# Optimization experiments

Hardware: AMD Instinct MI355X
Metric: run time of the kernel (lower is better)

Reference implementation:

```python
import jax, jax.numpy as jnp
import numpy as np
import math

B, C, H, W = 4, 256, 64, 64
N_GROUPS = 32
D_K = 64
N_HEADS = C // D_K  # 4
EPS = 1e-5


def setup_inputs() -> dict:
    key = jax.random.key(0)
    ks = jax.random.split(key, 7)
    return {
        "x": jax.random.normal(ks[0], (B, C, H, W), dtype=jnp.float32),
        "gamma": jax.random.uniform(ks[1], (C,), dtype=jnp.float32),
        "beta": jax.random.normal(ks[2], (C,), dtype=jnp.float32) * 0.1,
        "W_qkv": jax.random.normal(ks[3], (C, N_HEADS * D_K * 3), dtype=jnp.float32) * 0.02,
        "b_qkv": jax.random.normal(ks[4], (N_HEADS * D_K * 3,), dtype=jnp.float32) * 0.02,
        "W_out": jax.random.normal(ks[5], (N_HEADS * D_K, C), dtype=jnp.float32) * 0.02,
        "b_out": jax.random.normal(ks[6], (C,), dtype=jnp.float32) * 0.02,
    }


def _group_norm(x, gamma, beta):
    # x: [B, C, H, W], 32 groups, biased variance, eps=1e-5 (torch GroupNorm defaults)
    b, c, h, w = x.shape
    xg = x.reshape(b, N_GROUPS, c // N_GROUPS, h, w)
    mean = jnp.mean(xg, axis=(2, 3, 4), keepdims=True)
    var = jnp.var(xg, axis=(2, 3, 4), keepdims=True)
    xn = (xg - mean) / jnp.sqrt(var + EPS)
    xn = xn.reshape(b, c, h, w)
    return xn * gamma[None, :, None, None] + beta[None, :, None, None]


def reference(x, gamma, beta, W_qkv, b_qkv, W_out, b_out):
    b, c, h, w = x.shape
    n = h * w
    scale = 1.0 / math.sqrt(math.sqrt(D_K))
    # norm -> [B, N, C]
    hid = _group_norm(x, gamma, beta).reshape(b, c, n).transpose(0, 2, 1)
    # qkv projection -> [B, N, n_heads, 3*d_k], chunk on last dim
    qkv = (hid @ W_qkv + b_qkv).reshape(b, n, N_HEADS, 3 * D_K)
    q, k, v = jnp.split(qkv, 3, axis=-1)  # each [B, N, H, d_k]
    attn = jnp.einsum('bihd,bjhd->bijh', q * scale, k * scale)
    attn = jax.nn.softmax(attn, axis=2)  # softmax over j (keys)
    res = jnp.einsum('bijh,bjhd->bihd', attn, v).reshape(b, n, N_HEADS * D_K)
    res = res @ W_out + b_out  # [B, N, C]
    res = res.transpose(0, 2, 1).reshape(b, c, h, w)
    return (res + x) / math.sqrt(2.0)
```

## Files before the change

### kernel.cpp

```cpp
#include <hip/hip_runtime.h>
#include <math.h>

typedef float  f32x4   __attribute__((ext_vector_type(4)));
typedef float  f32x16  __attribute__((ext_vector_type(16)));
typedef __bf16 bf16x8  __attribute__((ext_vector_type(8)));
typedef __bf16 bf16x4  __attribute__((ext_vector_type(4)));

#define MFMA16(a, b, c) __builtin_amdgcn_mfma_f32_16x16x32_bf16((a), (b), (c), 0, 0, 0)
#define MFMA32(a, b, c) __builtin_amdgcn_mfma_f32_32x32x16_bf16((a), (b), (c), 0, 0, 0)

typedef __attribute__((address_space(3))) unsigned int lds_u32;
typedef __attribute__((address_space(1))) const unsigned int glb_u32;

__device__ __forceinline__ void gload16(const __bf16* g, char* l) {
    __builtin_amdgcn_global_load_lds((glb_u32*)g, (lds_u32*)l, 16, 0, 0);
}

static constexpr int BATCH = 4;
static constexpr int CH    = 256;
static constexpr int M_TOT = BATCH * 4096;

static constexpr float QSCALE = 0.18033688011112042f;

static constexpr size_t OFF_WQKV  = 0;
static constexpr size_t OFF_WOUT  = 196608ull * 2;
static constexpr size_t OFF_STATS = OFF_WOUT + 65536ull * 2;
static constexpr size_t OFF_HID   = OFF_STATS + 1024;
static constexpr size_t OFF_Q     = OFF_HID + (size_t)M_TOT * CH * 2;
static constexpr size_t OFF_K     = OFF_Q   + (size_t)M_TOT * CH * 2;
static constexpr size_t OFF_V     = OFF_K   + (size_t)M_TOT * CH * 2;

__global__ __launch_bounds__(256) void pre_kernel(const float* __restrict__ x,
                                                  float2* __restrict__ stats,
                                                  const float* __restrict__ wq,
                                                  const float* __restrict__ wo,
                                                  __bf16* __restrict__ wqf,
                                                  __bf16* __restrict__ wof) {
    if (blockIdx.x < 128) {
        int bg = blockIdx.x;
        const float4* p = (const float4*)(x + (size_t)bg * 32768);
        float s = 0.f, ss = 0.f;
        for (int i = threadIdx.x; i < 8192; i += 256) {
            float4 v = p[i];
            s  += (v.x + v.y) + (v.z + v.w);
            ss += v.x * v.x + v.y * v.y + v.z * v.z + v.w * v.w;
        }
#pragma unroll
        for (int d = 32; d > 0; d >>= 1) { s += __shfl_down(s, d); ss += __shfl_down(ss, d); }
        __shared__ float sh[8];
        int w = threadIdx.x >> 6, l = threadIdx.x & 63;
        if (l == 0) { sh[w] = s; sh[4 + w] = ss; }
        __syncthreads();
        if (threadIdx.x == 0) {
            float S = sh[0] + sh[1] + sh[2] + sh[3];
            float SS = sh[4] + sh[5] + sh[6] + sh[7];
            float mean = S * (1.f / 32768.f);
            float var  = SS * (1.f / 32768.f) - mean * mean;
            stats[bg] = make_float2(mean, rsqrtf(var + 1e-5f));
        }
    } else {
        int i = (blockIdx.x - 128) * 256 + threadIdx.x;
        if (i < 196608) {
            int e = i & 7, l = (i >> 3) & 63, kk = (i >> 9) & 7, jt = i >> 12;
            int kidx = kk * 32 + ((l >> 4) << 3) + e;
            int n = jt * 16 + (l & 15);
            wqf[i] = (__bf16)wq[kidx * 768 + n];
        } else {
            int i2 = i - 196608;
            int e = i2 & 7, l = (i2 >> 3) & 63, kk = (i2 >> 9) & 7, jt = i2 >> 12;
            int kidx = kk * 32 + ((l >> 4) << 3) + e;
            int n = jt * 16 + (l & 15);
            wof[i2] = (__bf16)wo[kidx * 256 + n];
        }
    }
}

__global__ __launch_bounds__(256) void gn_apply(const float* __restrict__ x,
                                                const float* __restrict__ gamma,
                                                const float* __restrict__ beta,
                                                const float2* __restrict__ stats,
                                                __bf16* __restrict__ hid) {
    int b  = blockIdx.x >> 6;
    int n0 = (blockIdx.x & 63) << 6;
    int c  = threadIdx.x;
    float2 st = stats[b * 32 + (c >> 3)];
    float gm = gamma[c] * st.y;
    float bt = beta[c] - st.x * gm;
    const float* xp = x + ((size_t)(b * 256 + c)) * 4096 + n0;
    __bf16* hp = hid + ((size_t)(b * 4096 + n0)) * 256 + c;
#pragma unroll
    for (int j4 = 0; j4 < 16; ++j4) {
        float4 v = *(const float4*)(xp + j4 * 4);
        hp[(size_t)(j4 * 4 + 0) * 256] = (__bf16)(v.x * gm + bt);
        hp[(size_t)(j4 * 4 + 1) * 256] = (__bf16)(v.y * gm + bt);
        hp[(size_t)(j4 * 4 + 2) * 256] = (__bf16)(v.z * gm + bt);
        hp[(size_t)(j4 * 4 + 3) * 256] = (__bf16)(v.w * gm + bt);
    }
}

__global__ __launch_bounds__(256) void qkv_gemm(const __bf16* __restrict__ hid,
                                                const __bf16* __restrict__ wf,
                                                const float* __restrict__ bqkv,
                                                __bf16* __restrict__ qb,
                                                __bf16* __restrict__ kb,
                                                __bf16* __restrict__ vb) {
    const int mt = blockIdx.x, nt = blockIdx.y;
    const int tid = threadIdx.x;
    const int w = tid >> 6, l = tid & 63;
    const int lr = l & 15, lh = l >> 4;
    f32x4 acc[4] = {{0.f,0.f,0.f,0.f},{0.f,0.f,0.f,0.f},{0.f,0.f,0.f,0.f},{0.f,0.f,0.f,0.f}};
    const __bf16* ap = hid + (size_t)(mt * 64 + w * 16 + lr) * 256 + lh * 8;
#pragma unroll
    for (int kk = 0; kk < 8; ++kk) {
        bf16x8 a = *(const bf16x8*)(ap + kk * 32);
#pragma unroll
        for (int fj = 0; fj < 4; ++fj) {
            bf16x8 bf = *(const bf16x8*)(wf + (size_t)(((nt * 4 + fj) * 8 + kk) * 64 + l) * 8);
            acc[fj] = MFMA16(a, bf, acc[fj]);
        }
    }
    const int part = nt % 3;
    const int head = nt / 3;
    const int b  = mt >> 6;
    const int n0 = (mt & 63) * 64;

    if (part == 2) {
        __shared__ float tile[64][72];
#pragma unroll
        for (int fj = 0; fj < 4; ++fj) {
            float bias = bqkv[head * 192 + 128 + fj * 16 + lr];
#pragma unroll
            for (int r = 0; r < 4; ++r)
                tile[w * 16 + lh * 4 + r][fj * 16 + lr] = acc[fj][r] + bias;
        }
        __syncthreads();
        int dd = tid >> 2, nq = tid & 3;
        __bf16* dstrow = vb + ((size_t)((b * 4 + head) * 64 + dd)) * 4096 + n0 + nq * 16;
        bf16x8 w0, w1;
#pragma unroll
        for (int cc = 0; cc < 8; ++cc) {
            int nl0 = nq * 16 + 8 * ((cc >> 2) & 1) + 4 * (cc >> 3) + (cc & 3);
            int cc1 = cc + 8;
            int nl1 = nq * 16 + 8 * ((cc1 >> 2) & 1) + 4 * (cc1 >> 3) + (cc1 & 3);
            w0[cc] = (__bf16)tile[nl0][dd];
            w1[cc] = (__bf16)tile[nl1][dd];
        }
        *(bf16x8*)dstrow = w0;
        *(bf16x8*)(dstrow + 8) = w1;
    } else {
        __bf16* dst = (part == 0) ? qb : kb;
        const float sc = (part == 0) ? QSCALE : 1.0f;
        int mbase = w * 16 + lh * 4;
#pragma unroll
        for (int fj = 0; fj < 4; ++fj) {
            int dd = fj * 16 + lr;
            float bias = bqkv[head * 192 + part * 64 + dd];
#pragma unroll
            for (int r = 0; r < 4; ++r) {
                int n = n0 + mbase + r;
                dst[((size_t)((b * 4 + head) * 4096 + n)) * 64 + dd] = (__bf16)((acc[fj][r] + bias) * sc);
            }
        }
    }
}

__global__ __launch_bounds__(256, 2) void attn_fwd(const __bf16* __restrict__ q,
                                                   const __bf16* __restrict__ k,
                                                   const __bf16* __restrict__ vt,
                                                   __bf16* __restrict__ ao) {
    const int id = blockIdx.x;
    const int within = id >> 3;
    const int bh = ((id & 7) << 1) + (within >> 5);
    const int q0 = (within & 31) * 128;
    const int tid = threadIdx.x;
    const int wv = tid >> 6, l = tid & 63;
    const int l31 = l & 31, h = l >> 5;

    __shared__ __attribute__((aligned(16))) char smem[32768];

    const size_t base = (size_t)bh * (4096 * 64);

    const int c0 = wv * 64 + l;
    const int rK = c0 >> 3, cbK = l & 7;
    const int gk0 = rK * 64 + (cbK ^ (rK & 7)) * 8;
    const int gk1 = gk0 + 2048;
    const int gv0 = rK * 4096 + (cbK ^ (rK & 7)) * 8;
    const int gv1 = gv0 + 32 * 4096;
    const int lw0 = wv * 1024;
    const int lw1 = 4096 + wv * 1024;

    const __bf16* kg = k + base;
    const __bf16* vg = vt + base;

    int foff[2][4];
#pragma unroll
    for (int b32 = 0; b32 < 2; ++b32) {
        int row = b32 * 32 + l31;
#pragma unroll
        for (int s = 0; s < 4; ++s)
            foff[b32][s] = row * 128 + ((s * 32 + h * 16) ^ ((row & 7) << 4));
    }

    bf16x8 qf[4];
    {
        const __bf16* qp = q + base + (size_t)(q0 + wv * 32 + l31) * 64 + h * 8;
#pragma unroll
        for (int ks = 0; ks < 4; ++ks) qf[ks] = *(const bf16x8*)(qp + ks * 16);
    }
    bf16x8 ones;
#pragma unroll
    for (int e = 0; e < 8; ++e) ones[e] = (__bf16)1.0f;

    f32x16 O0 = (f32x16)0.0f, O1 = (f32x16)0.0f, LS = (f32x16)0.0f;

    gload16(kg + gk0, smem + lw0);
    gload16(kg + gk1, smem + lw1);
    gload16(vg + gv0, smem + 16384 + lw0);
    gload16(vg + gv1, smem + 16384 + lw1);
    __syncthreads();

    auto body = [&](const char* Kc, const char* Vc, char* kd, char* vd, int tnext) {
        if (tnext < 64) {
            const __bf16* kp = kg + (size_t)tnext * 4096;
            const __bf16* vp = vg + (size_t)tnext * 64;
            gload16(kp + gk0, kd + lw0);
            gload16(kp + gk1, kd + lw1);
            gload16(vp + gv0, vd + lw0);
            gload16(vp + gv1, vd + lw1);
        }

        f32x16 S0 = (f32x16)0.0f, S1 = (f32x16)0.0f;
        __builtin_amdgcn_s_setprio(1);
#pragma unroll
        for (int ks = 0; ks < 4; ++ks) {
            bf16x8 ka0 = *(const bf16x8*)(Kc + foff[0][ks]);
            bf16x8 ka1 = *(const bf16x8*)(Kc + foff[1][ks]);
            S0 = MFMA32(ka0, qf[ks], S0);
            S1 = MFMA32(ka1, qf[ks], S1);
        }
        __builtin_amdgcn_s_setprio(0);

        bf16x8 B0, B1, B2, B3;
#pragma unroll
        for (int e = 0; e < 8; ++e) {
            B0[e] = (__bf16)__builtin_amdgcn_exp2f(S0[e]);
            B1[e] = (__bf16)__builtin_amdgcn_exp2f(S0[8 + e]);
            B2[e] = (__bf16)__builtin_amdgcn_exp2f(S1[e]);
            B3[e] = (__bf16)__builtin_amdgcn_exp2f(S1[8 + e]);
        }

        __builtin_amdgcn_s_setprio(1);
        {
            bf16x8 v00 = *(const bf16x8*)(Vc + foff[0][0]);
            bf16x8 v10 = *(const bf16x8*)(Vc + foff[1][0]);
            O0 = MFMA32(v00, B0, O0);
            O1 = MFMA32(v10, B0, O1);
            LS = MFMA32(ones, B0, LS);
            bf16x8 v01 = *(const bf16x8*)(Vc + foff[0][1]);
            bf16x8 v11 = *(const bf16x8*)(Vc + foff[1][1]);
            O0 = MFMA32(v01, B1, O0);
            O1 = MFMA32(v11, B1, O1);
            LS = MFMA32(ones, B1, LS);
            bf16x8 v02 = *(const bf16x8*)(Vc + foff[0][2]);
            bf16x8 v12 = *(const bf16x8*)(Vc + foff[1][2]);
            O0 = MFMA32(v02, B2, O0);
            O1 = MFMA32(v12, B2, O1);
            LS = MFMA32(ones, B2, LS);
            bf16x8 v03 = *(const bf16x8*)(Vc + foff[0][3]);
            bf16x8 v13 = *(const bf16x8*)(Vc + foff[1][3]);
            O0 = MFMA32(v03, B3, O0);
            O1 = MFMA32(v13, B3, O1);
            LS = MFMA32(ones, B3, LS);
        }
        __builtin_amdgcn_s_setprio(0);

        __syncthreads();
    };

    for (int t = 0; t < 64; t += 2) {
        body(smem,        smem + 16384,        smem + 8192, smem + 16384 + 8192, t + 1);
        body(smem + 8192, smem + 16384 + 8192, smem,        smem + 16384,        t + 2);
    }

    float inv = 1.0f / LS[0];
    int b = bh >> 2, hd = bh & 3;
    int n = q0 + wv * 32 + l31;
    __bf16* dst = ao + ((size_t)(b * 4096 + n)) * 256 + hd * 64 + h * 4;
#pragma unroll
    for (int dt = 0; dt < 2; ++dt) {
        const f32x16& O = dt ? O1 : O0;
#pragma unroll
        for (int g = 0; g < 4; ++g) {
            bf16x4 pk;
#pragma unroll
            for (int m = 0; m < 4; ++m) pk[m] = (__bf16)(O[g * 4 + m] * inv);
            *(bf16x4*)(dst + dt * 32 + g * 8) = pk;
        }
    }
}

__global__ __launch_bounds__(256) void out_gemm(const __bf16* __restrict__ ao,
                                                const __bf16* __restrict__ wf,
                                                const float* __restrict__ bout,
                                                const float* __restrict__ x,
                                                float* __restrict__ out) {
    const int mt = blockIdx.x, nt = blockIdx.y;
    const int tid = threadIdx.x;
    const int w = tid >> 6, l = tid & 63;
    const int lr = l & 15, lh = l >> 4;
    f32x4 acc[4] = {{0.f,0.f,0.f,0.f},{0.f,0.f,0.f,0.f},{0.f,0.f,0.f,0.f},{0.f,0.f,0.f,0.f}};
    const __bf16* ap = ao + (size_t)(mt * 64 + w * 16 + lr) * 256 + lh * 8;
#pragma unroll
    for (int kk = 0; kk < 8; ++kk) {
        bf16x8 a = *(const bf16x8*)(ap + kk * 32);
#pragma unroll
        for (int fj = 0; fj < 4; ++fj) {
            bf16x8 bf = *(const bf16x8*)(wf + (size_t)(((nt * 4 + fj) * 8 + kk) * 64 + l) * 8);
            acc[fj] = MFMA16(a, bf, acc[fj]);
        }
    }
    __shared__ float tile[64][72];
#pragma unroll
    for (int fj = 0; fj < 4; ++fj) {
        float bias = bout[nt * 64 + fj * 16 + lr];
#pragma unroll
        for (int r = 0; r < 4; ++r)
            tile[w * 16 + lh * 4 + r][fj * 16 + lr] = acc[fj][r] + bias;
    }
    __syncthreads();
    int b  = mt >> 6;
    int n0 = (mt & 63) * 64;
    int c0 = nt * 64;
    int cl = tid >> 2, nq = tid & 3;
    size_t gbase = ((size_t)(b * 256 + c0 + cl)) * 4096 + n0 + nq * 16;
#pragma unroll
    for (int i = 0; i < 16; i += 4) {
        float4 xv = *(const float4*)(x + gbase + i);
        float4 ov;
        ov.x = (tile[nq * 16 + i + 0][cl] + xv.x) * 0.70710678118654752f;
        ov.y = (tile[nq * 16 + i + 1][cl] + xv.y) * 0.70710678118654752f;
        ov.z = (tile[nq * 16 + i + 2][cl] + xv.z) * 0.70710678118654752f;
        ov.w = (tile[nq * 16 + i + 3][cl] + xv.w) * 0.70710678118654752f;
        *(float4*)(out + gbase + i) = ov;
    }
}

extern "C" void kernel_launch(void* const* d_in, const int* in_sizes, int n_in,
                              void* d_out, int out_size, void* d_ws, size_t ws_size,
                              hipStream_t stream) {
    const float* x     = (const float*)d_in[0];
    const float* gamma = (const float*)d_in[1];
    const float* beta  = (const float*)d_in[2];
    const float* W_qkv = (const float*)d_in[3];
    const float* b_qkv = (const float*)d_in[4];
    const float* W_out = (const float*)d_in[5];
    const float* b_out = (const float*)d_in[6];
    float* out = (float*)d_out;
    char* ws = (char*)d_ws;

    __bf16* wqf   = (__bf16*)(ws + OFF_WQKV);
    __bf16* wof   = (__bf16*)(ws + OFF_WOUT);
    float2* stats = (float2*)(ws + OFF_STATS);
    __bf16* hid   = (__bf16*)(ws + OFF_HID);
    __bf16* qb    = (__bf16*)(ws + OFF_Q);
    __bf16* kb    = (__bf16*)(ws + OFF_K);
    __bf16* vbt   = (__bf16*)(ws + OFF_V);

    pre_kernel<<<1152, 256, 0, stream>>>(x, stats, W_qkv, W_out, wqf, wof);
    gn_apply<<<256, 256, 0, stream>>>(x, gamma, beta, stats, hid);
    qkv_gemm<<<dim3(256, 12), 256, 0, stream>>>(hid, wqf, b_qkv, qb, kb, vbt);
    attn_fwd<<<512, 256, 0, stream>>>(qb, kb, vbt, hid);
    out_gemm<<<dim3(256, 4), 256, 0, stream>>>(hid, wof, b_out, x, out);
}
```

Baseline: 144.4 us.

## Split attention key range across wave pairs and merge partial outputs in LDS

Each attention block now handles 64 queries instead of 128. Its four waves form two pairs, and each pair processes half of the keys with its own double-buffered K/V tiles. The launch doubles to 1024 blocks with a larger occupancy target, and the ones-matrix MFMA row sum is replaced by scalar accumulation of the exponentials. At the end, partial O and row sums are reduced through shared memory. This trades more blocks and an extra LDS reduction step for more parallelism and fewer MFMAs per tile, and it drops the LDS swizzle, which may add bank conflicts.

```diff
diff --git a/kernel.cpp b/kernel.cpp
--- a/kernel.cpp
+++ b/kernel.cpp
@@ -164,137 +164,130 @@
     }
 }
 
-__global__ __launch_bounds__(256, 2) void attn_fwd(const __bf16* __restrict__ q,
+__global__ __launch_bounds__(256, 4) void attn_fwd(const __bf16* __restrict__ q,
                                                    const __bf16* __restrict__ k,
                                                    const __bf16* __restrict__ vt,
                                                    __bf16* __restrict__ ao) {
     const int id = blockIdx.x;
     const int within = id >> 3;
-    const int bh = ((id & 7) << 1) + (within >> 5);
-    const int q0 = (within & 31) * 128;
+    const int bh = ((id & 7) << 1) + (within >> 6);
+    const int q0 = (within & 63) * 64;
     const int tid = threadIdx.x;
     const int wv = tid >> 6, l = tid & 63;
     const int l31 = l & 31, h = l >> 5;
+    const int pair = wv >> 1;
+    const int wq   = wv & 1;
 
     __shared__ __attribute__((aligned(16))) char smem[32768];
 
     const size_t base = (size_t)bh * (4096 * 64);
-
-    const int c0 = wv * 64 + l;
-    const int rK = c0 >> 3, cbK = l & 7;
-    const int gk0 = rK * 64 + (cbK ^ (rK & 7)) * 8;
-    const int gk1 = gk0 + 2048;
-    const int gv0 = rK * 4096 + (cbK ^ (rK & 7)) * 8;
-    const int gv1 = gv0 + 32 * 4096;
-    const int lw0 = wv * 1024;
-    const int lw1 = 4096 + wv * 1024;
-
     const __bf16* kg = k + base;
     const __bf16* vg = vt + base;
 
-    int foff[2][4];
-#pragma unroll
-    for (int b32 = 0; b32 < 2; ++b32) {
-        int row = b32 * 32 + l31;
-#pragma unroll
-        for (int s = 0; s < 4; ++s)
-            foff[b32][s] = row * 128 + ((s * 32 + h * 16) ^ ((row & 7) << 4));
-    }
+    const int kS0 = (l & 31) * 64 + wq * 16 + (l >> 5) * 8;
+    const int kS1 = kS0 + 32;
+    const int vS0 = (l & 31) * 4096 + wq * 16 + (l >> 5) * 8;
+    const int vS1 = vS0 + 32 * 4096;
+    const int dst0 = wq * 1024 + l * 16;
+    const int dst1 = dst0 + 2048;
+    const int pairBase = pair * 16384;
+    const int kTileStride = 2048;
+    const int pairKeyElemsK = pair * 131072;
+    const int pairColV = pair * 2048;
 
     bf16x8 qf[4];
     {
-        const __bf16* qp = q + base + (size_t)(q0 + wv * 32 + l31) * 64 + h * 8;
+        const __bf16* qp = q + base + (size_t)(q0 + wq * 32 + l31) * 64 + h * 8;
 #pragma unroll
         for (int ks = 0; ks < 4; ++ks) qf[ks] = *(const bf16x8*)(qp + ks * 16);
     }
-    bf16x8 ones;
-#pragma unroll
-    for (int e = 0; e < 8; ++e) ones[e] = (__bf16)1.0f;
-
-    f32x16 O0 = (f32x16)0.0f, O1 = (f32x16)0.0f, LS = (f32x16)0.0f;
-
-    gload16(kg + gk0, smem + lw0);
-    gload16(kg + gk1, smem + lw1);
-    gload16(vg + gv0, smem + 16384 + lw0);
-    gload16(vg + gv1, smem + 16384 + lw1);
+
+    f32x16 O0 = (f32x16)0.0f, O1 = (f32x16)0.0f;
+    float ls = 0.f;
+
+    gload16(kg + pairKeyElemsK + kS0, smem + pairBase + dst0);
+    gload16(kg + pairKeyElemsK + kS1, smem + pairBase + dst1);
+    gload16(vg + pairColV + vS0, smem + pairBase + 8192 + dst0);
+    gload16(vg + pairColV + vS1, smem + pairBase + 8192 + dst1);
     __syncthreads();
 
-    auto body = [&](const char* Kc, const char* Vc, char* kd, char* vd, int tnext) {
+    auto body = [&](int buf, int tnext) {
         if (tnext < 64) {
-            const __bf16* kp = kg + (size_t)tnext * 4096;
-            const __bf16* vp = vg + (size_t)tnext * 64;
-            gload16(kp + gk0, kd + lw0);
-            gload16(kp + gk1, kd + lw1);
-            gload16(vp + gv0, vd + lw0);
-            gload16(vp + gv1, vd + lw1);
-        }
-
-        f32x16 S0 = (f32x16)0.0f, S1 = (f32x16)0.0f;
+            const __bf16* kp = kg + pairKeyElemsK + tnext * kTileStride;
+            const __bf16* vp = vg + pairColV + tnext * 32;
+            char* kd = smem + pairBase + (buf ^ 1) * 4096;
+            char* vd = smem + pairBase + 8192 + (buf ^ 1) * 4096;
+            gload16(kp + kS0, kd + dst0);
+            gload16(kp + kS1, kd + dst1);
+            gload16(vp + vS0, vd + dst0);
+            gload16(vp + vS1, vd + dst1);
+        }
+        const char* Kl = smem + pairBase + buf * 4096 + l * 16;
+        const char* Vl = smem + pairBase + 8192 + buf * 4096 + l * 16;
+
+        f32x16 S = (f32x16)0.0f;
         __builtin_amdgcn_s_setprio(1);
 #pragma unroll
-        for (int ks = 0; ks < 4; ++ks) {
-            bf16x8 ka0 = *(const bf16x8*)(Kc + foff[0][ks]);
-            bf16x8 ka1 = *(const bf16x8*)(Kc + foff[1][ks]);
-            S0 = MFMA32(ka0, qf[ks], S0);
-            S1 = MFMA32(ka1, qf[ks], S1);
-        }
+        for (int ks = 0; ks < 4; ++ks)
+            S = MFMA32(*(const bf16x8*)(Kl + ks * 1024), qf[ks], S);
         __builtin_amdgcn_s_setprio(0);
 
-        bf16x8 B0, B1, B2, B3;
+        bf16x8 B0, B1;
 #pragma unroll
         for (int e = 0; e < 8; ++e) {
-            B0[e] = (__bf16)__builtin_amdgcn_exp2f(S0[e]);
-            B1[e] = (__bf16)__builtin_amdgcn_exp2f(S0[8 + e]);
-            B2[e] = (__bf16)__builtin_amdgcn_exp2f(S1[e]);
-            B3[e] = (__bf16)__builtin_amdgcn_exp2f(S1[8 + e]);
+            float p0 = __builtin_amdgcn_exp2f(S[e]);
+            float p1 = __builtin_amdgcn_exp2f(S[8 + e]);
+            ls += p0 + p1;
+            B0[e] = (__bf16)p0;
+            B1[e] = (__bf16)p1;
         }
 
         __builtin_amdgcn_s_setprio(1);
-        {
-            bf16x8 v00 = *(const bf16x8*)(Vc + foff[0][0]);
-            bf16x8 v10 = *(const bf16x8*)(Vc + foff[1][0]);
-            O0 = MFMA32(v00, B0, O0);
-            O1 = MFMA32(v10, B0, O1);
-            LS = MFMA32(ones, B0, LS);
-            bf16x8 v01 = *(const bf16x8*)(Vc + foff[0][1]);
-            bf16x8 v11 = *(const bf16x8*)(Vc + foff[1][1]);
-            O0 = MFMA32(v01, B1, O0);
-            O1 = MFMA32(v11, B1, O1);
-            LS = MFMA32(ones, B1, LS);
-            bf16x8 v02 = *(const bf16x8*)(Vc + foff[0][2]);
-            bf16x8 v12 = *(const bf16x8*)(Vc + foff[1][2]);
-            O0 = MFMA32(v02, B2, O0);
-            O1 = MFMA32(v12, B2, O1);
-            LS = MFMA32(ones, B2, LS);
-            bf16x8 v03 = *(const bf16x8*)(Vc + foff[0][3]);
-            bf16x8 v13 = *(const bf16x8*)(Vc + foff[1][3]);
-            O0 = MFMA32(v03, B3, O0);
-            O1 = MFMA32(v13, B3, O1);
-            LS = MFMA32(ones, B3, LS);
-        }
+        O0 = MFMA32(*(const bf16x8*)(Vl + 0),    B0, O0);
+        O0 = MFMA32(*(const bf16x8*)(Vl + 1024), B1, O0);
+        O1 = MFMA32(*(const bf16x8*)(Vl + 2048), B0, O1);
+        O1 = MFMA32(*(const bf16x8*)(Vl + 3072), B1, O1);
         __builtin_amdgcn_s_setprio(0);
 
         __syncthreads();
     };
 
     for (int t = 0; t < 64; t += 2) {
-        body(smem,        smem + 16384,        smem + 8192, smem + 16384 + 8192, t + 1);
-        body(smem + 8192, smem + 16384 + 8192, smem,        smem + 16384,        t + 2);
-    }
-
-    float inv = 1.0f / LS[0];
-    int b = bh >> 2, hd = bh & 3;
-    int n = q0 + wv * 32 + l31;
-    __bf16* dst = ao + ((size_t)(b * 4096 + n)) * 256 + hd * 64 + h * 4;
-#pragma unroll
-    for (int dt = 0; dt < 2; ++dt) {
-        const f32x16& O = dt ? O1 : O0;
-#pragma unroll
-        for (int g = 0; g < 4; ++g) {
-            bf16x4 pk;
-#pragma unroll
-            for (int m = 0; m < 4; ++m) pk[m] = (__bf16)(O[g * 4 + m] * inv);
-            *(bf16x4*)(dst + dt * 32 + g * 8) = pk;
+        body(0, t + 1);
+        body(1, t + 2);
+    }
+
+    if (wv >= 2) {
+        float* d = (float*)(smem + ((wv - 2) * 64 + l) * 144);
+        const f32x4* o0p = (const f32x4*)&O0;
+        const f32x4* o1p = (const f32x4*)&O1;
+#pragma unroll
+        for (int i = 0; i < 4; ++i) ((f32x4*)d)[i] = o0p[i];
+#pragma unroll
+        for (int i = 0; i < 4; ++i) ((f32x4*)(d + 16))[i] = o1p[i];
+        d[32] = ls;
+    }
+    __syncthreads();
+    if (wv < 2) {
+        const float* s = (const float*)(smem + (wv * 64 + l) * 144);
+#pragma unroll
+        for (int j = 0; j < 16; ++j) { O0[j] += s[j]; O1[j] += s[16 + j]; }
+        ls += s[32];
+        ls += __shfl_xor(ls, 32);
+        float inv = 1.0f / ls;
+        int b = bh >> 2, hd = bh & 3;
+        int n = q0 + wv * 32 + l31;
+        __bf16* dst = ao + ((size_t)(b * 4096 + n)) * 256 + hd * 64 + h * 4;
+#pragma unroll
+        for (int dt = 0; dt < 2; ++dt) {
+            const f32x16& O = dt ? O1 : O0;
+#pragma unroll
+            for (int g = 0; g < 4; ++g) {
+                bf16x4 pk;
+#pragma unroll
+                for (int m = 0; m < 4; ++m) pk[m] = (__bf16)(O[g * 4 + m] * inv);
+                *(bf16x4*)(dst + dt * 32 + g * 8) = pk;
+            }
         }
     }
 }
@@ -369,6 +362,6 @@
     pre_kernel<<<1152, 256, 0, stream>>>(x, stats, W_qkv, W_out, wqf, wof);
     gn_apply<<<256, 256, 0, stream>>>(x, gamma, beta, stats, hid);
     qkv_gemm<<<dim3(256, 12), 256, 0, stream>>>(hid, wqf, b_qkv, qb, kb, vbt);
-    attn_fwd<<<512, 256, 0, stream>>>(qb, kb, vbt, hid);
+    attn_fwd<<<1024, 256, 0, stream>>>(qb, kb, vbt, hid);
     out_gemm<<<dim3(256, 4), 256, 0, stream>>>(hid, wof, b_out, x, out);
 }
```

New measurement: 191.6 us. 1.33x slower.
